# Performance work log

Measured on AMD Instinct MI355X. Metric: run time of the kernel, lower is better.

## Reference

```python
import jax, jax.numpy as jnp
import numpy as np

LUT_N = 16 * 17 * 17 * 17  # 78608, covers max index 16*(16*17*17 + 16*17 + 16) = 78592
H = W = 2048


def setup_inputs() -> dict:
    key = jax.random.key(0)
    k1, k2, k3, k4 = jax.random.split(key, 4)
    # quantized pixel values in [0, 16], stored as float like the torch module expects
    x_in = jax.random.randint(k1, (1, 3, H, W), 0, 17).astype(jnp.float32)
    x_s = jax.random.randint(k2, (1, 3, H, W), 0, 17).astype(jnp.float32)
    # int8 LUT tables of shape [N, 20, 1, 1]
    feature_msb = jax.random.randint(k3, (LUT_N, 20, 1, 1), -32, 32).astype(jnp.int8)
    feature_lsb = jax.random.randint(k4, (LUT_N, 20, 1, 1), -32, 32).astype(jnp.int8)
    return {"x_in": x_in, "x_s": x_s, "feature_msb": feature_msb, "feature_lsb": feature_lsb}


def reference(x_in, x_s, feature_msb, feature_lsb):
    B, C, Hh, Ww = x_in.shape
    # index weights: [16*17*17, 16*17, 16], broadcast over (1,3,1,1)
    weights = jnp.array([16 * 17 * 17, 16 * 17, 16], dtype=jnp.float32).reshape(1, 3, 1, 1)
    idx_msb = jnp.sum(x_in * weights, axis=1).reshape(-1).astype(jnp.int32)  # [B*H*W]
    idx_lsb = jnp.sum(x_s * weights, axis=1).reshape(-1).astype(jnp.int32)
    nfeat = feature_msb.shape[1]  # 20
    # gather -> (1, H, W, 20) -> (1, 20, H, W), cast to float as in torch .float()
    out_msb = feature_msb[idx_msb].reshape(1, Hh, Ww, nfeat).transpose(0, 3, 1, 2).astype(jnp.float32)
    out_lsb = feature_lsb[idx_lsb].reshape(1, Hh, Ww, nfeat).transpose(0, 3, 1, 2).astype(jnp.float32)
    out = out_msb + out_lsb
    # AdaptiveAvgPool2d(1) == global mean over H, W
    out = jnp.mean(out, axis=(2, 3), keepdims=True)  # (1, 20, 1, 1)
    # quantize to 0.25 steps and clamp to [-32, 31.75]
    out = jnp.clip(jnp.round(out * 4.0) / 4.0, -32.0, 31.75)
    return out
```

## Files before the change

### kernel.cpp

```cpp
#include <hip/hip_runtime.h>


#define NBINS 4913
#define HPAD  4928
#define NPIX  (2048 * 2048)
#define G4    (NPIX / 4)
#define NFEAT 20
#define NH    1024
#define HT    512
#define BINGRP 154
#define ROWGRP 16

#define PART_OFF 196608
#define HIST_OFF 458752

__device__ __forceinline__ void compact_range(const int* __restrict__ msb,
                                              const int* __restrict__ lsb,
                                              int* __restrict__ cm,
                                              int* __restrict__ cl,
                                              int t0, int stride) {
    int ok = 1;
    for (int i = 0; i < 64; ++i) {
        int v = msb[i];
        ok &= (v >= -32 && v < 32);
    }
    const bool is_int32 = (ok != 0);

    const int total = NBINS * 5;
    for (int t = t0; t < total; t += stride) {
        int j = t / 5;
        int k = t - j * 5;
        int wm, wl;
        if (is_int32) {
            const int* rm = msb + j * 320 + k * 4;
            const int* rl = lsb + j * 320 + k * 4;
            unsigned um = (unsigned)(rm[0] & 0xff) | ((unsigned)(rm[1] & 0xff) << 8) |
                          ((unsigned)(rm[2] & 0xff) << 16) | ((unsigned)(rm[3] & 0xff) << 24);
            unsigned ul = (unsigned)(rl[0] & 0xff) | ((unsigned)(rl[1] & 0xff) << 8) |
                          ((unsigned)(rl[2] & 0xff) << 16) | ((unsigned)(rl[3] & 0xff) << 24);
            wm = (int)um;
            wl = (int)ul;
        } else {
            wm = msb[j * 80 + k];
            wl = lsb[j * 80 + k];
        }
        cm[t] = wm;
        cl[t] = wl;
    }
}

__global__ __launch_bounds__(HT) void feat_hist(const float* __restrict__ xin,
                                                const float* __restrict__ xs,
                                                const int* __restrict__ msb,
                                                const int* __restrict__ lsb,
                                                int* __restrict__ cm,
                                                int* __restrict__ cl,
                                                unsigned* __restrict__ hists) {
    __shared__ int hist[NBINS];
    for (int i = threadIdx.x; i < NBINS; i += HT) hist[i] = 0;

    if (blockIdx.x < 48)
        compact_range(msb, lsb, cm, cl, blockIdx.x * HT + threadIdx.x, 48 * HT);
    __syncthreads();

    const float4* a = (const float4*)xin;
    const float4* b = (const float4*)xs;
    const int nt = gridDim.x * HT;
    for (int g = blockIdx.x * HT + threadIdx.x; g < G4; g += nt) {
        float4 a0 = a[g], a1 = a[g + G4], a2 = a[g + 2 * G4];
        float4 b0 = b[g], b1 = b[g + G4], b2 = b[g + 2 * G4];

        int m0 = (int)fmaf(a0.x, 289.0f, fmaf(a1.x, 17.0f, a2.x));
        int m1 = (int)fmaf(a0.y, 289.0f, fmaf(a1.y, 17.0f, a2.y));
        int m2 = (int)fmaf(a0.z, 289.0f, fmaf(a1.z, 17.0f, a2.z));
        int m3 = (int)fmaf(a0.w, 289.0f, fmaf(a1.w, 17.0f, a2.w));
        int s0 = (int)fmaf(b0.x, 289.0f, fmaf(b1.x, 17.0f, b2.x));
        int s1 = (int)fmaf(b0.y, 289.0f, fmaf(b1.y, 17.0f, b2.y));
        int s2 = (int)fmaf(b0.z, 289.0f, fmaf(b1.z, 17.0f, b2.z));
        int s3 = (int)fmaf(b0.w, 289.0f, fmaf(b1.w, 17.0f, b2.w));

        atomicAdd(&hist[m0], 1);
        atomicAdd(&hist[m1], 1);
        atomicAdd(&hist[m2], 1);
        atomicAdd(&hist[m3], 1);
        atomicAdd(&hist[s0], 1 << 16);
        atomicAdd(&hist[s1], 1 << 16);
        atomicAdd(&hist[s2], 1 << 16);
        atomicAdd(&hist[s3], 1 << 16);
    }
    __syncthreads();

    unsigned* row = hists + (size_t)blockIdx.x * HPAD;
    for (int i = threadIdx.x; i < HPAD; i += HT)
        row[i] = (i < NBINS) ? (unsigned)hist[i] : 0u;
}

__global__ __launch_bounds__(256) void merge_dot_k(const unsigned* __restrict__ hists,
                                                   const int* __restrict__ cm,
                                                   const int* __restrict__ cl,
                                                   int* __restrict__ partial) {
    __shared__ unsigned part[8][32];
    const int t = threadIdx.x;
    const int s = t >> 5;
    const int bo = t & 31;
    const int j = blockIdx.x * 32 + bo;

    const int rpg = NH / ROWGRP;
    const int r0 = blockIdx.y * rpg;
    const int r1 = r0 + rpg;

    unsigned sum = 0;
    for (int b = r0 + s; b < r1; b += 8)
        sum += hists[(size_t)b * HPAD + j];
    part[s][bo] = sum;
    __syncthreads();

    if (t < 32) {
        unsigned h = 0;
#pragma unroll
        for (int ss = 0; ss < 8; ++ss) h += part[ss][bo];
        int hm = (int)(h & 0xffffu);
        int hl = (int)(h >> 16);

        int acc[NFEAT];
#pragma unroll
        for (int f = 0; f < NFEAT; ++f) acc[f] = 0;
        if (j < NBINS && h != 0u) {
            const int* rm = cm + j * 5;
            const int* rl = cl + j * 5;
#pragma unroll
            for (int k = 0; k < 5; ++k) {
                int wm = rm[k], wl = rl[k];
                acc[4 * k + 0] += hm * ((wm << 24) >> 24) + hl * ((wl << 24) >> 24);
                acc[4 * k + 1] += hm * ((wm << 16) >> 24) + hl * ((wl << 16) >> 24);
                acc[4 * k + 2] += hm * ((wm << 8) >> 24) + hl * ((wl << 8) >> 24);
                acc[4 * k + 3] += hm * (wm >> 24) + hl * (wl >> 24);
            }
        }
#pragma unroll
        for (int f = 0; f < NFEAT; ++f) {
            int v = acc[f];
#pragma unroll
            for (int o = 16; o > 0; o >>= 1) v += __shfl_xor(v, o, 64);
            acc[f] = v;
        }
        if (t == 0) {
            const int row = blockIdx.y * BINGRP + blockIdx.x;
#pragma unroll
            for (int f = 0; f < NFEAT; ++f)
                partial[row * NFEAT + f] = acc[f];
        }
    }
}

__global__ __launch_bounds__(256) void compact_k(const int* __restrict__ msb,
                                                 const int* __restrict__ lsb,
                                                 int* __restrict__ cm,
                                                 int* __restrict__ cl) {
    compact_range(msb, lsb, cm, cl, blockIdx.x * 256 + threadIdx.x, gridDim.x * 256);
}

__global__ __launch_bounds__(256) void feat_dot(const float* __restrict__ xin,
                                                const float* __restrict__ xs,
                                                const int* __restrict__ cm,
                                                const int* __restrict__ cl,
                                                int* __restrict__ partial) {
    __shared__ int hist[NBINS];
    __shared__ int wsum[4][NFEAT];
    for (int i = threadIdx.x; i < NBINS; i += 256) hist[i] = 0;
    __syncthreads();

    const float4* a = (const float4*)xin;
    const float4* b = (const float4*)xs;
    const int nt = gridDim.x * 256;
    for (int g = blockIdx.x * 256 + threadIdx.x; g < G4; g += nt) {
        float4 a0 = a[g], a1 = a[g + G4], a2 = a[g + 2 * G4];
        float4 b0 = b[g], b1 = b[g + G4], b2 = b[g + 2 * G4];
        int m0 = (int)fmaf(a0.x, 289.0f, fmaf(a1.x, 17.0f, a2.x));
        int m1 = (int)fmaf(a0.y, 289.0f, fmaf(a1.y, 17.0f, a2.y));
        int m2 = (int)fmaf(a0.z, 289.0f, fmaf(a1.z, 17.0f, a2.z));
        int m3 = (int)fmaf(a0.w, 289.0f, fmaf(a1.w, 17.0f, a2.w));
        int s0 = (int)fmaf(b0.x, 289.0f, fmaf(b1.x, 17.0f, b2.x));
        int s1 = (int)fmaf(b0.y, 289.0f, fmaf(b1.y, 17.0f, b2.y));
        int s2 = (int)fmaf(b0.z, 289.0f, fmaf(b1.z, 17.0f, b2.z));
        int s3 = (int)fmaf(b0.w, 289.0f, fmaf(b1.w, 17.0f, b2.w));
        atomicAdd(&hist[m0], 1);
        atomicAdd(&hist[m1], 1);
        atomicAdd(&hist[m2], 1);
        atomicAdd(&hist[m3], 1);
        atomicAdd(&hist[s0], 1 << 16);
        atomicAdd(&hist[s1], 1 << 16);
        atomicAdd(&hist[s2], 1 << 16);
        atomicAdd(&hist[s3], 1 << 16);
    }
    __syncthreads();

    int acc[NFEAT];
#pragma unroll
    for (int f = 0; f < NFEAT; ++f) acc[f] = 0;
    for (int j = threadIdx.x; j < NBINS; j += 256) {
        int h = hist[j];
        int hm = h & 0xffff;
        int hl = (int)((unsigned)h >> 16);
        if (hm) {
            const int* r = cm + j * 5;
#pragma unroll
            for (int k = 0; k < 5; ++k) {
                int w = r[k];
                acc[4 * k + 0] += hm * ((w << 24) >> 24);
                acc[4 * k + 1] += hm * ((w << 16) >> 24);
                acc[4 * k + 2] += hm * ((w << 8) >> 24);
                acc[4 * k + 3] += hm * (w >> 24);
            }
        }
        if (hl) {
            const int* r = cl + j * 5;
#pragma unroll
            for (int k = 0; k < 5; ++k) {
                int w = r[k];
                acc[4 * k + 0] += hl * ((w << 24) >> 24);
                acc[4 * k + 1] += hl * ((w << 16) >> 24);
                acc[4 * k + 2] += hl * ((w << 8) >> 24);
                acc[4 * k + 3] += hl * (w >> 24);
            }
        }
    }

    const int lane = threadIdx.x & 63;
    const int wv = threadIdx.x >> 6;
#pragma unroll
    for (int f = 0; f < NFEAT; ++f) {
        int v = acc[f];
#pragma unroll
        for (int o = 32; o > 0; o >>= 1) v += __shfl_xor(v, o, 64);
        if (lane == 0) wsum[wv][f] = v;
    }
    __syncthreads();
    if (threadIdx.x < NFEAT) {
        int f = threadIdx.x;
        partial[blockIdx.x * NFEAT + f] = wsum[0][f] + wsum[1][f] + wsum[2][f] + wsum[3][f];
    }
}

__global__ __launch_bounds__(64) void finalize_k(const int* __restrict__ partial,
                                                 float* __restrict__ out, int nb) {
    const int f = blockIdx.x;
    const int lane = threadIdx.x;
    int s = 0;
    for (int b = lane; b < nb; b += 64) s += partial[b * NFEAT + f];
#pragma unroll
    for (int o = 32; o > 0; o >>= 1) s += __shfl_xor(s, o, 64);
    if (lane == 0) {
        double m4 = (double)s * (1.0 / 1048576.0);
        double r = rint(m4);
        float v = (float)(r * 0.25);
        v = fminf(fmaxf(v, -32.0f), 31.75f);
        out[f] = v;
    }
}

extern "C" void kernel_launch(void* const* d_in, const int* in_sizes, int n_in,
                              void* d_out, int out_size, void* d_ws, size_t ws_size,
                              hipStream_t stream) {
    const float* xin = (const float*)d_in[0];
    const float* xs = (const float*)d_in[1];
    const int* msb = (const int*)d_in[2];
    const int* lsb = (const int*)d_in[3];
    float* out = (float*)d_out;

    int* cm = (int*)d_ws;
    int* cl = (int*)((char*)d_ws + 98304);
    int* partial = (int*)((char*)d_ws + PART_OFF);
    unsigned* hists = (unsigned*)((char*)d_ws + HIST_OFF);

    const size_t need = (size_t)HIST_OFF + (size_t)NH * HPAD * 4;
    if (ws_size >= need) {
        feat_hist<<<NH, HT, 0, stream>>>(xin, xs, msb, lsb, cm, cl, hists);
        merge_dot_k<<<dim3(BINGRP, ROWGRP), 256, 0, stream>>>(hists, cm, cl, partial);
        finalize_k<<<NFEAT, 64, 0, stream>>>(partial, out, BINGRP * ROWGRP);
    } else {
        compact_k<<<96, 256, 0, stream>>>(msb, lsb, cm, cl);
        feat_dot<<<1024, 256, 0, stream>>>(xin, xs, cm, cl, partial);
        finalize_k<<<NFEAT, 64, 0, stream>>>(partial, out, 1024);
    }
}
```

Measured before the change: 149.8 us.

## Halve histogram grid and issue all global loads upfront with staged waitcnts

```diff
diff --git a/kernel.cpp b/kernel.cpp
--- a/kernel.cpp
+++ b/kernel.cpp
@@ -6,7 +6,7 @@
 #define NPIX  (2048 * 2048)
 #define G4    (NPIX / 4)
 #define NFEAT 20
-#define NH    1024
+#define NH    512
 #define HT    512
 #define BINGRP 154
 #define ROWGRP 16
@@ -49,6 +49,25 @@
     }
 }
 
+#define GLOAD(dst, addr)                                                    \
+    asm volatile("global_load_dwordx4 %0, %1, off" : "=&v"(dst) : "v"(addr) : "memory")
+
+#define IDX4(d, v0, v1, v2)                                      \
+    int d##0 = (int)fmaf(v0.x, 289.0f, fmaf(v1.x, 17.0f, v2.x)); \
+    int d##1 = (int)fmaf(v0.y, 289.0f, fmaf(v1.y, 17.0f, v2.y)); \
+    int d##2 = (int)fmaf(v0.z, 289.0f, fmaf(v1.z, 17.0f, v2.z)); \
+    int d##3 = (int)fmaf(v0.w, 289.0f, fmaf(v1.w, 17.0f, v2.w));
+
+#define HIST8(m, s)                 \
+    atomicAdd(&hist[m##0], 1);      \
+    atomicAdd(&hist[m##1], 1);      \
+    atomicAdd(&hist[m##2], 1);      \
+    atomicAdd(&hist[m##3], 1);      \
+    atomicAdd(&hist[s##0], 1 << 16);\
+    atomicAdd(&hist[s##1], 1 << 16);\
+    atomicAdd(&hist[s##2], 1 << 16);\
+    atomicAdd(&hist[s##3], 1 << 16);
+
 __global__ __launch_bounds__(HT) void feat_hist(const float* __restrict__ xin,
                                                 const float* __restrict__ xs,
                                                 const int* __restrict__ msb,
@@ -63,31 +82,40 @@
         compact_range(msb, lsb, cm, cl, blockIdx.x * HT + threadIdx.x, 48 * HT);
     __syncthreads();
 
-    const float4* a = (const float4*)xin;
-    const float4* b = (const float4*)xs;
-    const int nt = gridDim.x * HT;
-    for (int g = blockIdx.x * HT + threadIdx.x; g < G4; g += nt) {
-        float4 a0 = a[g], a1 = a[g + G4], a2 = a[g + 2 * G4];
-        float4 b0 = b[g], b1 = b[g + G4], b2 = b[g + 2 * G4];
-
-        int m0 = (int)fmaf(a0.x, 289.0f, fmaf(a1.x, 17.0f, a2.x));
-        int m1 = (int)fmaf(a0.y, 289.0f, fmaf(a1.y, 17.0f, a2.y));
-        int m2 = (int)fmaf(a0.z, 289.0f, fmaf(a1.z, 17.0f, a2.z));
-        int m3 = (int)fmaf(a0.w, 289.0f, fmaf(a1.w, 17.0f, a2.w));
-        int s0 = (int)fmaf(b0.x, 289.0f, fmaf(b1.x, 17.0f, b2.x));
-        int s1 = (int)fmaf(b0.y, 289.0f, fmaf(b1.y, 17.0f, b2.y));
-        int s2 = (int)fmaf(b0.z, 289.0f, fmaf(b1.z, 17.0f, b2.z));
-        int s3 = (int)fmaf(b0.w, 289.0f, fmaf(b1.w, 17.0f, b2.w));
-
-        atomicAdd(&hist[m0], 1);
-        atomicAdd(&hist[m1], 1);
-        atomicAdd(&hist[m2], 1);
-        atomicAdd(&hist[m3], 1);
-        atomicAdd(&hist[s0], 1 << 16);
-        atomicAdd(&hist[s1], 1 << 16);
-        atomicAdd(&hist[s2], 1 << 16);
-        atomicAdd(&hist[s3], 1 << 16);
-    }
+    const int tid = blockIdx.x * HT + threadIdx.x;
+    const unsigned long long nt16 = (unsigned long long)(NH * HT) * 16ull;
+    unsigned long long pa = (unsigned long long)xin + (unsigned long long)tid * 16ull;
+    unsigned long long pb = (unsigned long long)xs + (unsigned long long)tid * 16ull;
+    const unsigned long long P = (unsigned long long)G4 * 16ull;
+
+    float4 A00, A01, A02, B00, B01, B02;
+    float4 A10, A11, A12, B10, B11, B12;
+    float4 A20, A21, A22, B20, B21, B22;
+    float4 A30, A31, A32, B30, B31, B32;
+    GLOAD(A00, pa); GLOAD(A01, pa + P); GLOAD(A02, pa + 2 * P);
+    GLOAD(B00, pb); GLOAD(B01, pb + P); GLOAD(B02, pb + 2 * P);
+    pa += nt16; pb += nt16;
+    GLOAD(A10, pa); GLOAD(A11, pa + P); GLOAD(A12, pa + 2 * P);
+    GLOAD(B10, pb); GLOAD(B11, pb + P); GLOAD(B12, pb + 2 * P);
+    pa += nt16; pb += nt16;
+    GLOAD(A20, pa); GLOAD(A21, pa + P); GLOAD(A22, pa + 2 * P);
+    GLOAD(B20, pb); GLOAD(B21, pb + P); GLOAD(B22, pb + 2 * P);
+    pa += nt16; pb += nt16;
+    GLOAD(A30, pa); GLOAD(A31, pa + P); GLOAD(A32, pa + 2 * P);
+    GLOAD(B30, pb); GLOAD(B31, pb + P); GLOAD(B32, pb + 2 * P);
+
+    asm volatile("s_waitcnt vmcnt(18)" ::: "memory");
+    __builtin_amdgcn_sched_barrier(0);
+    { IDX4(m, A00, A01, A02) IDX4(s, B00, B01, B02) HIST8(m, s) }
+    asm volatile("s_waitcnt vmcnt(12)" ::: "memory");
+    __builtin_amdgcn_sched_barrier(0);
+    { IDX4(m, A10, A11, A12) IDX4(s, B10, B11, B12) HIST8(m, s) }
+    asm volatile("s_waitcnt vmcnt(6)" ::: "memory");
+    __builtin_amdgcn_sched_barrier(0);
+    { IDX4(m, A20, A21, A22) IDX4(s, B20, B21, B22) HIST8(m, s) }
+    asm volatile("s_waitcnt vmcnt(0)" ::: "memory");
+    __builtin_amdgcn_sched_barrier(0);
+    { IDX4(m, A30, A31, A32) IDX4(s, B30, B31, B32) HIST8(m, s) }
     __syncthreads();
 
     unsigned* row = hists + (size_t)blockIdx.x * HPAD;
@@ -176,22 +204,9 @@
     for (int g = blockIdx.x * 256 + threadIdx.x; g < G4; g += nt) {
         float4 a0 = a[g], a1 = a[g + G4], a2 = a[g + 2 * G4];
         float4 b0 = b[g], b1 = b[g + G4], b2 = b[g + 2 * G4];
-        int m0 = (int)fmaf(a0.x, 289.0f, fmaf(a1.x, 17.0f, a2.x));
-        int m1 = (int)fmaf(a0.y, 289.0f, fmaf(a1.y, 17.0f, a2.y));
-        int m2 = (int)fmaf(a0.z, 289.0f, fmaf(a1.z, 17.0f, a2.z));
-        int m3 = (int)fmaf(a0.w, 289.0f, fmaf(a1.w, 17.0f, a2.w));
-        int s0 = (int)fmaf(b0.x, 289.0f, fmaf(b1.x, 17.0f, b2.x));
-        int s1 = (int)fmaf(b0.y, 289.0f, fmaf(b1.y, 17.0f, b2.y));
-        int s2 = (int)fmaf(b0.z, 289.0f, fmaf(b1.z, 17.0f, b2.z));
-        int s3 = (int)fmaf(b0.w, 289.0f, fmaf(b1.w, 17.0f, b2.w));
-        atomicAdd(&hist[m0], 1);
-        atomicAdd(&hist[m1], 1);
-        atomicAdd(&hist[m2], 1);
-        atomicAdd(&hist[m3], 1);
-        atomicAdd(&hist[s0], 1 << 16);
-        atomicAdd(&hist[s1], 1 << 16);
-        atomicAdd(&hist[s2], 1 << 16);
-        atomicAdd(&hist[s3], 1 << 16);
+        IDX4(m, a0, a1, a2)
+        IDX4(s, b0, b1, b2)
+        HIST8(m, s)
     }
     __syncthreads();
 
```

Measured after the change: 149.0 us. Within noise of the previous version (-0.6%).
